# Kernel tuning notes

Measured on AMD Instinct MI355X. Metric: run time of the kernel, lower is better.

The kernel has to match this reference:

```python
import jax, jax.numpy as jnp
import numpy as np

NUM_GRAPHS = 1000


def _gine_conv(x, src, dst, edge_attr, w_e, b_e, w1, b1, w2, b2):
    # GINEConv (eps=0): out = nn(x + sum_{j->i} relu(x_j + lin_edge(e_ji)))
    e = edge_attr @ w_e + b_e                      # [E, F]
    m = jax.nn.relu(x[src] + e)                    # [E, F] per-edge message
    agg = jnp.zeros_like(x).at[dst].add(m)         # [N, F] scatter-add to targets
    h = x + agg
    h = jax.nn.relu(h @ w1 + b1)
    h = jax.nn.relu(h @ w2 + b2)
    return h


def _segment_softmax(scores, seg, num_segments):
    m = jax.ops.segment_max(scores, seg, num_segments=num_segments)
    z = jnp.exp(scores - m[seg])
    s = jax.ops.segment_sum(z, seg, num_segments=num_segments)
    return z / s[seg]


def setup_inputs() -> dict:
    key = jax.random.key(0)
    ks = jax.random.split(key, 16)
    N, E, F_IN, H, ED = 100000, 1600000, 9, 64, 1

    x = jax.random.normal(ks[0], (N, F_IN), dtype=jnp.float32)
    edge_index = jax.random.randint(ks[1], (2, E), 0, N, dtype=jnp.int32)
    edge_attr = jax.random.normal(ks[2], (E, ED), dtype=jnp.float32)
    batch = jnp.sort(jax.random.randint(ks[3], (N,), 0, NUM_GRAPHS, dtype=jnp.int32))
    B_total = jax.random.uniform(ks[4], (NUM_GRAPHS,), dtype=jnp.float32)

    def lin(k, fi, fo):
        k1, k2 = jax.random.split(k)
        bound = 1.0 / np.sqrt(fi)
        w = jax.random.uniform(k1, (fi, fo), minval=-bound, maxval=bound, dtype=jnp.float32)
        b = jax.random.uniform(k2, (fo,), minval=-bound, maxval=bound, dtype=jnp.float32)
        return w, b

    we1, be1 = lin(ks[5], ED, F_IN)    # conv1 edge projection -> in_channels
    w11, b11 = lin(ks[6], F_IN, H)
    w12, b12 = lin(ks[7], H, H)
    we2, be2 = lin(ks[8], ED, H)       # conv2 edge projection
    w21, b21 = lin(ks[9], H, H)
    w22, b22 = lin(ks[10], H, H)
    wr1, br1 = lin(ks[11], H, H // 2)
    wr2, br2 = lin(ks[12], H // 2, 1)

    return {"x": x, "edge_index": edge_index, "edge_attr": edge_attr,
            "batch": batch, "B_total": B_total,
            "we1": we1, "be1": be1, "w11": w11, "b11": b11, "w12": w12, "b12": b12,
            "we2": we2, "be2": be2, "w21": w21, "b21": b21, "w22": w22, "b22": b22,
            "wr1": wr1, "br1": br1, "wr2": wr2, "br2": br2}


def reference(x, edge_index, edge_attr, batch, B_total,
              we1, be1, w11, b11, w12, b12,
              we2, be2, w21, b21, w22, b22,
              wr1, br1, wr2, br2):
    src, dst = edge_index[0], edge_index[1]
    h = _gine_conv(x, src, dst, edge_attr, we1, be1, w11, b11, w12, b12)
    h = _gine_conv(h, src, dst, edge_attr, we2, be2, w21, b21, w22, b22)
    raw = (jax.nn.relu(h @ wr1 + br1) @ wr2 + br2)[:, 0]   # [N]
    alloc_probs = _segment_softmax(raw, batch, NUM_GRAPHS)
    return alloc_probs * B_total[batch]
```

## Files before the change

### kernel.cpp

```cpp
#include <hip/hip_runtime.h>
#include <float.h>

__global__ void deg_rank_kernel(const int* __restrict__ dst, int* __restrict__ deg,
                                int* __restrict__ rank, int E) {
  int j = blockIdx.x * blockDim.x + threadIdx.x;
  if (j < E) rank[j] = atomicAdd(&deg[dst[j]], 1);
}

__global__ void scan_pass1(const int* __restrict__ deg, int* __restrict__ blocksum, int N) {
  __shared__ int sdata[1024];
  int i = blockIdx.x * 1024 + threadIdx.x;
  sdata[threadIdx.x] = (i < N) ? deg[i] : 0;
  __syncthreads();
  for (int s = 512; s > 0; s >>= 1) {
    if (threadIdx.x < s) sdata[threadIdx.x] += sdata[threadIdx.x + s];
    __syncthreads();
  }
  if (threadIdx.x == 0) blocksum[blockIdx.x] = sdata[0];
}

__global__ void scan_pass2(int* __restrict__ blocksum, int nb) {
  __shared__ int sdata[1024];
  int t = threadIdx.x;
  sdata[t] = (t < nb) ? blocksum[t] : 0;
  __syncthreads();
  if (t == 0) {
    int run = 0;
    for (int i = 0; i < nb; ++i) { int v = sdata[i]; sdata[i] = run; run += v; }
  }
  __syncthreads();
  if (t < nb) blocksum[t] = sdata[t];
}

__global__ void scan_pass3(const int* __restrict__ deg, const int* __restrict__ blocksum,
                           int* __restrict__ rowptr, int N, int E) {
  __shared__ int sdata[1024];
  int i = blockIdx.x * 1024 + threadIdx.x;
  int v = (i < N) ? deg[i] : 0;
  sdata[threadIdx.x] = v;
  __syncthreads();
  for (int off = 1; off < 1024; off <<= 1) {
    int t = (threadIdx.x >= off) ? sdata[threadIdx.x - off] : 0;
    __syncthreads();
    sdata[threadIdx.x] += t;
    __syncthreads();
  }
  if (i < N) rowptr[i] = blocksum[blockIdx.x] + sdata[threadIdx.x] - v;
  if (i == 0) rowptr[N] = E;
}

__global__ void scatter_kernel(const int* __restrict__ dst, const int* __restrict__ rank,
                               const int* __restrict__ rowptr,
                               const int* __restrict__ src, const float* __restrict__ ea,
                               int2* __restrict__ epack, int E) {
  int j = blockIdx.x * blockDim.x + threadIdx.x;
  if (j >= E) return;
  int pos = rowptr[dst[j]] + rank[j];
  epack[pos] = make_int2(src[j], __float_as_int(ea[j]));
}

__global__ void __launch_bounds__(256, 8) gather1_kernel(
    const float* __restrict__ x, const int* __restrict__ rowptr,
    const int2* __restrict__ epack,
    const float* __restrict__ we1, const float* __restrict__ be1,
    float* __restrict__ xin, int N) {
  int i = blockIdx.x * blockDim.x + threadIdx.x;
  if (i >= N) return;
  float we[9], be[9];
#pragma unroll
  for (int f = 0; f < 9; ++f) { we[f] = we1[f]; be[f] = be1[f]; }
  float acc[9];
#pragma unroll
  for (int f = 0; f < 9; ++f) acc[f] = 0.0f;

  int p0 = rowptr[i], p1 = rowptr[i + 1];
  int p = p0;
  for (; p + 1 < p1; p += 2) {
    int2 e0 = epack[p], e1 = epack[p + 1];
    float a0 = __int_as_float(e0.y), a1 = __int_as_float(e1.y);
    float r0[9], r1[9];
#pragma unroll
    for (int f = 0; f < 9; ++f) r0[f] = x[(size_t)e0.x * 9 + f];
#pragma unroll
    for (int f = 0; f < 9; ++f) r1[f] = x[(size_t)e1.x * 9 + f];
#pragma unroll
    for (int f = 0; f < 9; ++f) {
      acc[f] += fmaxf(fmaf(a0, we[f], be[f]) + r0[f], 0.0f);
      acc[f] += fmaxf(fmaf(a1, we[f], be[f]) + r1[f], 0.0f);
    }
  }
  for (; p < p1; ++p) {
    int2 e = epack[p];
    float a = __int_as_float(e.y);
#pragma unroll
    for (int f = 0; f < 9; ++f)
      acc[f] += fmaxf(fmaf(a, we[f], be[f]) + x[(size_t)e.x * 9 + f], 0.0f);
  }
#pragma unroll
  for (int f = 0; f < 9; ++f) xin[(size_t)i * 9 + f] = x[(size_t)i * 9 + f] + acc[f];
}

__global__ void __launch_bounds__(256, 3) node1_mlp(
    const float* __restrict__ xin,
    const float* __restrict__ w11, const float* __restrict__ b11,
    const float* __restrict__ w12, const float* __restrict__ b12,
    float* __restrict__ h1, unsigned short* __restrict__ h1b, int N) {
  __shared__ float sW1[9 * 64];
  __shared__ float sB1[64];
  __shared__ float sW2[64 * 64];
  __shared__ float sB2[64];
  for (int t = threadIdx.x; t < 9 * 64; t += blockDim.x) sW1[t] = w11[t];
  for (int t = threadIdx.x; t < 64; t += blockDim.x) { sB1[t] = b11[t]; sB2[t] = b12[t]; }
  for (int t = threadIdx.x; t < 64 * 64; t += blockDim.x) sW2[t] = w12[t];
  __syncthreads();
  int i = blockIdx.x * blockDim.x + threadIdx.x;
  if (i >= N) return;
  float xv[9];
#pragma unroll
  for (int k = 0; k < 9; ++k) xv[k] = xin[(size_t)i * 9 + k];
  float t1[64];
#pragma unroll
  for (int o = 0; o < 64; ++o) {
    float a = sB1[o];
#pragma unroll
    for (int k = 0; k < 9; ++k) a = fmaf(xv[k], sW1[k * 64 + o], a);
    t1[o] = fmaxf(a, 0.0f);
  }
  for (int o = 0; o < 64; ++o) {
    float a = sB2[o];
#pragma unroll
    for (int k = 0; k < 64; ++k) a = fmaf(t1[k], sW2[k * 64 + o], a);
    float v = fmaxf(a, 0.0f);
    h1[(size_t)i * 64 + o] = v;
    unsigned u = __float_as_uint(v);
    h1b[(size_t)i * 64 + o] = (unsigned short)((u + 0x7FFFu + ((u >> 16) & 1u)) >> 16);
  }
}

__device__ __forceinline__ float4 bf4_to_f4(uint2 u) {
  float4 r;
  r.x = __uint_as_float(u.x << 16);
  r.y = __uint_as_float(u.x & 0xFFFF0000u);
  r.z = __uint_as_float(u.y << 16);
  r.w = __uint_as_float(u.y & 0xFFFF0000u);
  return r;
}

__global__ void __launch_bounds__(256, 8) gather2_kernel(
    const unsigned short* __restrict__ h1b, const int* __restrict__ rowptr,
    const int2* __restrict__ epack,
    const float* __restrict__ we2, const float* __restrict__ be2,
    float* __restrict__ agg2, int N) {
  int wid = threadIdx.x >> 6;
  int lane = threadIdx.x & 63;
  int g = lane >> 4;
  int l = lane & 15;
  int i = blockIdx.x * 4 + wid;
  if (i >= N) return;

  float4 we_l = *(const float4*)(we2 + 4 * l);
  float4 be_l = *(const float4*)(be2 + 4 * l);
  float4 acc = make_float4(0.f, 0.f, 0.f, 0.f);

  int p0 = rowptr[i], p1 = rowptr[i + 1];
  int p = p0 + g;
  for (; p + 4 < p1; p += 8) {
    int2 e0 = epack[p], e1 = epack[p + 4];
    float a0 = __int_as_float(e0.y), a1 = __int_as_float(e1.y);
    float4 h0 = bf4_to_f4(*(const uint2*)(h1b + (size_t)e0.x * 64 + 4 * l));
    float4 hv = bf4_to_f4(*(const uint2*)(h1b + (size_t)e1.x * 64 + 4 * l));
    acc.x += fmaxf(fmaf(a0, we_l.x, be_l.x) + h0.x, 0.f);
    acc.y += fmaxf(fmaf(a0, we_l.y, be_l.y) + h0.y, 0.f);
    acc.z += fmaxf(fmaf(a0, we_l.z, be_l.z) + h0.z, 0.f);
    acc.w += fmaxf(fmaf(a0, we_l.w, be_l.w) + h0.w, 0.f);
    acc.x += fmaxf(fmaf(a1, we_l.x, be_l.x) + hv.x, 0.f);
    acc.y += fmaxf(fmaf(a1, we_l.y, be_l.y) + hv.y, 0.f);
    acc.z += fmaxf(fmaf(a1, we_l.z, be_l.z) + hv.z, 0.f);
    acc.w += fmaxf(fmaf(a1, we_l.w, be_l.w) + hv.w, 0.f);
  }
  for (; p < p1; p += 4) {
    int2 e = epack[p];
    float a = __int_as_float(e.y);
    float4 h = bf4_to_f4(*(const uint2*)(h1b + (size_t)e.x * 64 + 4 * l));
    acc.x += fmaxf(fmaf(a, we_l.x, be_l.x) + h.x, 0.f);
    acc.y += fmaxf(fmaf(a, we_l.y, be_l.y) + h.y, 0.f);
    acc.z += fmaxf(fmaf(a, we_l.z, be_l.z) + h.z, 0.f);
    acc.w += fmaxf(fmaf(a, we_l.w, be_l.w) + h.w, 0.f);
  }
#pragma unroll
  for (int off = 16; off <= 32; off <<= 1) {
    acc.x += __shfl_xor(acc.x, off);
    acc.y += __shfl_xor(acc.y, off);
    acc.z += __shfl_xor(acc.z, off);
    acc.w += __shfl_xor(acc.w, off);
  }
  if (g == 0) *(float4*)(agg2 + (size_t)i * 64 + 4 * l) = acc;
}

__global__ void __launch_bounds__(256, 3) node2_kernel(
    const float* __restrict__ h1, const float* __restrict__ agg2,
    const float* __restrict__ w21, const float* __restrict__ b21,
    const float* __restrict__ w22, const float* __restrict__ b22,
    const float* __restrict__ wr1, const float* __restrict__ br1,
    const float* __restrict__ wr2, const float* __restrict__ br2,
    float* __restrict__ raw, int N) {
  __shared__ float sW1[64 * 64];
  __shared__ float sB1[64];
  __shared__ float sW2[64 * 64];
  __shared__ float sB2[64];
  __shared__ float sWr1[64 * 32];
  __shared__ float sBr1[32];
  __shared__ float sWr2[32];
  __shared__ float sBr2;
  for (int t = threadIdx.x; t < 64 * 64; t += blockDim.x) { sW1[t] = w21[t]; sW2[t] = w22[t]; }
  for (int t = threadIdx.x; t < 64; t += blockDim.x) { sB1[t] = b21[t]; sB2[t] = b22[t]; }
  for (int t = threadIdx.x; t < 64 * 32; t += blockDim.x) sWr1[t] = wr1[t];
  for (int t = threadIdx.x; t < 32; t += blockDim.x) { sBr1[t] = br1[t]; sWr2[t] = wr2[t]; }
  if (threadIdx.x == 0) sBr2 = br2[0];
  __syncthreads();
  int i = blockIdx.x * blockDim.x + threadIdx.x;
  if (i >= N) return;
  float hin[64];
#pragma unroll
  for (int k = 0; k < 64; ++k) hin[k] = h1[(size_t)i * 64 + k] + agg2[(size_t)i * 64 + k];
  float a1[64];
#pragma unroll
  for (int o = 0; o < 64; ++o) {
    float acc = sB1[o];
#pragma unroll
    for (int k = 0; k < 64; ++k) acc = fmaf(hin[k], sW1[k * 64 + o], acc);
    a1[o] = fmaxf(acc, 0.0f);
  }
  float a2[64];
#pragma unroll
  for (int o = 0; o < 64; ++o) {
    float acc = sB2[o];
#pragma unroll
    for (int k = 0; k < 64; ++k) acc = fmaf(a1[k], sW2[k * 64 + o], acc);
    a2[o] = fmaxf(acc, 0.0f);
  }
  float r[32];
#pragma unroll
  for (int o = 0; o < 32; ++o) {
    float acc = sBr1[o];
#pragma unroll
    for (int k = 0; k < 64; ++k) acc = fmaf(a2[k], sWr1[k * 32 + o], acc);
    r[o] = fmaxf(acc, 0.0f);
  }
  float acc = sBr2;
#pragma unroll
  for (int k = 0; k < 32; ++k) acc = fmaf(r[k], sWr2[k], acc);
  raw[i] = acc;
}

__device__ __forceinline__ int lowerb(const int* __restrict__ a, int n, int key) {
  int lo = 0, hi = n;
  while (lo < hi) { int mid = (lo + hi) >> 1; if (a[mid] < key) lo = mid + 1; else hi = mid; }
  return lo;
}

__global__ void segsoftmax_kernel(const float* __restrict__ raw, const int* __restrict__ batch,
                                  const float* __restrict__ Btot, float* __restrict__ out, int N) {
  __shared__ float sred[256];
  int g = blockIdx.x;
  int tid = threadIdx.x;
  int start = lowerb(batch, N, g);
  int end = lowerb(batch, N, g + 1);
  if (start >= end) return;

  float m = -FLT_MAX;
  for (int i = start + tid; i < end; i += 256) m = fmaxf(m, raw[i]);
  sred[tid] = m;
  __syncthreads();
  for (int s = 128; s > 0; s >>= 1) {
    if (tid < s) sred[tid] = fmaxf(sred[tid], sred[tid + s]);
    __syncthreads();
  }
  m = sred[0];
  __syncthreads();

  float sum = 0.0f;
  for (int i = start + tid; i < end; i += 256) sum += expf(raw[i] - m);
  sred[tid] = sum;
  __syncthreads();
  for (int s = 128; s > 0; s >>= 1) {
    if (tid < s) sred[tid] += sred[tid + s];
    __syncthreads();
  }
  float scale = Btot[g] / sred[0];

  for (int i = start + tid; i < end; i += 256) out[i] = expf(raw[i] - m) * scale;
}

extern "C" void kernel_launch(void* const* d_in, const int* in_sizes, int n_in,
                              void* d_out, int out_size, void* d_ws, size_t ws_size,
                              hipStream_t stream) {
  const float* x     = (const float*)d_in[0];
  const int* eidx    = (const int*)d_in[1];
  const float* eattr = (const float*)d_in[2];
  const int* batch   = (const int*)d_in[3];
  const float* Btot  = (const float*)d_in[4];
  const float* we1 = (const float*)d_in[5];
  const float* be1 = (const float*)d_in[6];
  const float* w11 = (const float*)d_in[7];
  const float* b11 = (const float*)d_in[8];
  const float* w12 = (const float*)d_in[9];
  const float* b12 = (const float*)d_in[10];
  const float* we2 = (const float*)d_in[11];
  const float* be2 = (const float*)d_in[12];
  const float* w21 = (const float*)d_in[13];
  const float* b21 = (const float*)d_in[14];
  const float* w22 = (const float*)d_in[15];
  const float* b22 = (const float*)d_in[16];
  const float* wr1 = (const float*)d_in[17];
  const float* br1 = (const float*)d_in[18];
  const float* wr2 = (const float*)d_in[19];
  const float* br2 = (const float*)d_in[20];

  const int N  = in_sizes[0] / 9;
  const int E  = in_sizes[2];
  const int NG = in_sizes[4];
  const int* src = eidx;
  const int* dst = eidx + E;

  const int NB = (N + 1023) / 1024;

  char* w = (char*)d_ws;
  int*   deg    = (int*)w;                 w += (size_t)N * 4;
  int*   rowptr = (int*)w;                 w += (size_t)(N + 1) * 4;
  int*   blocksum = (int*)w;               w += (size_t)1024 * 4;
  int*   rank   = (int*)w;                 w += (size_t)E * 4;
  int2*  epack  = (int2*)w;                w += (size_t)E * 8;
  float* h1     = (float*)w;               w += (size_t)N * 64 * 4;
  unsigned short* h1b = (unsigned short*)w; w += (size_t)N * 64 * 2;
  float* agg2   = (float*)w;               w += (size_t)N * 64 * 4;
  float* raw    = (float*)w;               w += (size_t)N * 4;
  float* xin = agg2;

  hipMemsetAsync(deg, 0, (size_t)N * 4, stream);

  dim3 blk(256);
  dim3 egrid((E + 255) / 256);
  dim3 ngrid((N + 255) / 256);

  deg_rank_kernel<<<egrid, blk, 0, stream>>>(dst, deg, rank, E);
  scan_pass1<<<dim3(NB), dim3(1024), 0, stream>>>(deg, blocksum, N);
  scan_pass2<<<dim3(1), dim3(1024), 0, stream>>>(blocksum, NB);
  scan_pass3<<<dim3(NB), dim3(1024), 0, stream>>>(deg, blocksum, rowptr, N, E);
  scatter_kernel<<<egrid, blk, 0, stream>>>(dst, rank, rowptr, src, eattr, epack, E);

  gather1_kernel<<<ngrid, blk, 0, stream>>>(x, rowptr, epack, we1, be1, xin, N);
  node1_mlp<<<ngrid, blk, 0, stream>>>(xin, w11, b11, w12, b12, h1, h1b, N);

  dim3 l2grid((N + 3) / 4);
  gather2_kernel<<<l2grid, blk, 0, stream>>>(h1b, rowptr, epack, we2, be2, agg2, N);
  node2_kernel<<<ngrid, blk, 0, stream>>>(h1, agg2, w21, b21, w22, b22,
                                          wr1, br1, wr2, br2, raw, N);

  segsoftmax_kernel<<<dim3(NG), blk, 0, stream>>>(raw, batch, Btot, (float*)d_out, N);
}
```

Measured before the change: 342.1 us.

## Store node1 output feature-major and add bf16 pack-transpose kernel

```diff
diff --git a/kernel.cpp b/kernel.cpp
--- a/kernel.cpp
+++ b/kernel.cpp
@@ -104,7 +104,7 @@
     const float* __restrict__ xin,
     const float* __restrict__ w11, const float* __restrict__ b11,
     const float* __restrict__ w12, const float* __restrict__ b12,
-    float* __restrict__ h1, unsigned short* __restrict__ h1b, int N) {
+    float* __restrict__ h1t, int N) {
   __shared__ float sW1[9 * 64];
   __shared__ float sB1[64];
   __shared__ float sW2[64 * 64];
@@ -130,10 +130,37 @@
     float a = sB2[o];
 #pragma unroll
     for (int k = 0; k < 64; ++k) a = fmaf(t1[k], sW2[k * 64 + o], a);
-    float v = fmaxf(a, 0.0f);
-    h1[(size_t)i * 64 + o] = v;
+    h1t[(size_t)o * N + i] = fmaxf(a, 0.0f);
+  }
+}
+
+__global__ void __launch_bounds__(256) pack_kernel(
+    const float* __restrict__ h1t, unsigned short* __restrict__ h1b, int N) {
+  __shared__ unsigned short tile[64][72];
+  int i0 = blockIdx.x * 64;
+  int l = threadIdx.x & 63;
+  int q = threadIdx.x >> 6;
+  int node = i0 + l;
+#pragma unroll
+  for (int it = 0; it < 16; ++it) {
+    int o = it * 4 + q;
+    float v = (node < N) ? h1t[(size_t)o * N + node] : 0.0f;
     unsigned u = __float_as_uint(v);
-    h1b[(size_t)i * 64 + o] = (unsigned short)((u + 0x7FFFu + ((u >> 16) & 1u)) >> 16);
+    tile[l][o] = (unsigned short)((u + 0x7FFFu + ((u >> 16) & 1u)) >> 16);
+  }
+  __syncthreads();
+#pragma unroll
+  for (int it = 0; it < 4; ++it) {
+    int idx = it * 256 + threadIdx.x;
+    int r = idx >> 4;
+    int c = idx & 15;
+    if (i0 + r < N) {
+      const unsigned short* tp = &tile[r][c * 4];
+      uint2 v;
+      v.x = (unsigned)tp[0] | ((unsigned)tp[1] << 16);
+      v.y = (unsigned)tp[2] | ((unsigned)tp[3] << 16);
+      *(uint2*)(h1b + (size_t)(i0 + r) * 64 + c * 4) = v;
+    }
   }
 }
 
@@ -198,7 +225,7 @@
 }
 
 __global__ void __launch_bounds__(256, 3) node2_kernel(
-    const float* __restrict__ h1, const float* __restrict__ agg2,
+    const float* __restrict__ h1t, const float* __restrict__ agg2,
     const float* __restrict__ w21, const float* __restrict__ b21,
     const float* __restrict__ w22, const float* __restrict__ b22,
     const float* __restrict__ wr1, const float* __restrict__ br1,
@@ -222,7 +249,8 @@
   if (i >= N) return;
   float hin[64];
 #pragma unroll
-  for (int k = 0; k < 64; ++k) hin[k] = h1[(size_t)i * 64 + k] + agg2[(size_t)i * 64 + k];
+  for (int k = 0; k < 64; ++k)
+    hin[k] = h1t[(size_t)k * N + i] + agg2[(size_t)i * 64 + k];
   float a1[64];
 #pragma unroll
   for (int o = 0; o < 64; ++o) {
@@ -331,7 +359,7 @@
   int*   blocksum = (int*)w;               w += (size_t)1024 * 4;
   int*   rank   = (int*)w;                 w += (size_t)E * 4;
   int2*  epack  = (int2*)w;                w += (size_t)E * 8;
-  float* h1     = (float*)w;               w += (size_t)N * 64 * 4;
+  float* h1t    = (float*)w;               w += (size_t)N * 64 * 4;
   unsigned short* h1b = (unsigned short*)w; w += (size_t)N * 64 * 2;
   float* agg2   = (float*)w;               w += (size_t)N * 64 * 4;
   float* raw    = (float*)w;               w += (size_t)N * 4;
@@ -350,11 +378,12 @@
   scatter_kernel<<<egrid, blk, 0, stream>>>(dst, rank, rowptr, src, eattr, epack, E);
 
   gather1_kernel<<<ngrid, blk, 0, stream>>>(x, rowptr, epack, we1, be1, xin, N);
-  node1_mlp<<<ngrid, blk, 0, stream>>>(xin, w11, b11, w12, b12, h1, h1b, N);
+  node1_mlp<<<ngrid, blk, 0, stream>>>(xin, w11, b11, w12, b12, h1t, N);
+  pack_kernel<<<dim3((N + 63) / 64), blk, 0, stream>>>(h1t, h1b, N);
 
   dim3 l2grid((N + 3) / 4);
   gather2_kernel<<<l2grid, blk, 0, stream>>>(h1b, rowptr, epack, we2, be2, agg2, N);
-  node2_kernel<<<ngrid, blk, 0, stream>>>(h1, agg2, w21, b21, w22, b22,
+  node2_kernel<<<ngrid, blk, 0, stream>>>(h1t, agg2, w21, b21, w22, b22,
                                           wr1, br1, wr2, br2, raw, N);
 
   segsoftmax_kernel<<<dim3(NG), blk, 0, stream>>>(raw, batch, Btot, (float*)d_out, N);
```

Result: faster. 318.4 us (-6.9%).
